# Optimization experiments

Hardware: AMD Instinct MI355X
Metric: run time of the kernel (lower is better)

The kernel has to match this reference:

```python
import jax, jax.numpy as jnp
import numpy as np

CLASS_W = jnp.array([0.3, 3.0, 0.3], dtype=jnp.float32)
GAMMA = 2.0
DICE_SMOOTH = 1.0
SKEL_SMOOTH = 1.0
W_FD, W_SK, W_B = 0.3, 0.3, 0.2
BIG = 1e8  # > max possible squared distance (3*63^2), keeps values finite


def _sq_edt(feature):
    """Exact squared Euclidean distance to nearest True voxel, separable
    per-axis (Felzenszwalb-style lower envelope realized as a brute-force
    min over each line, fully vectorized). feature: bool [B,D,H,W]."""
    d2 = jnp.where(feature, 0.0, BIG).astype(jnp.float32)
    for ax in range(1, d2.ndim):
        L = d2.shape[ax]
        i = jnp.arange(L, dtype=jnp.float32)
        cost = (i[:, None] - i[None, :]) ** 2  # [L, L]
        m = jnp.moveaxis(d2, ax, -1)           # [..., L]
        m = jnp.min(m[..., None, :] + cost, axis=-1)
        d2 = jnp.moveaxis(m, -1, ax)
    return d2


def setup_inputs() -> dict:
    key = jax.random.key(0)
    k1, k2, k3 = jax.random.split(key, 3)
    logits = jax.random.normal(k1, (4, 3, 64, 64, 64), dtype=jnp.float32)
    targets = jax.random.randint(k2, (4, 64, 64, 64), 0, 3, dtype=jnp.int64)
    skeleton = jax.random.randint(k3, (4, 64, 64, 64), 0, 2, dtype=jnp.int32)
    return {"logits": logits, "targets": targets, "skeleton": skeleton}


def reference(logits, targets, skeleton):
    num_classes = logits.shape[1]
    log_p = jax.nn.log_softmax(logits, axis=1)
    probs = jnp.exp(log_p)

    # ---- focal loss ----
    tgt = targets[:, None]  # [B,1,D,H,W]
    p_t = jnp.take_along_axis(probs, tgt, axis=1)[:, 0]
    log_p_t = jnp.take_along_axis(log_p, tgt, axis=1)[:, 0]
    alpha_t = CLASS_W[targets]
    focal = -(alpha_t * (1.0 - p_t) ** GAMMA * log_p_t).mean()

    # ---- dice loss (weighted, per class) ----
    dice = 0.0
    for c in range(num_classes):
        p = probs[:, c]
        t = (targets == c).astype(jnp.float32)
        inter = (p * t).sum()
        union = p.sum() + t.sum()
        dice = dice + CLASS_W[c] * (1.0 - (2.0 * inter + DICE_SMOOTH) / (union + DICE_SMOOTH))
    lfd = focal + dice / CLASS_W.sum()

    # ---- skeleton recall ----
    pred = probs[:, 1]  # surface class
    skel = skeleton.astype(jnp.float32)
    lsk = 1.0 - ((pred * skel).sum() + SKEL_SMOOTH) / (skel.sum() + SKEL_SMOOTH)

    # ---- boundary (signed distance transform) loss ----
    gt = targets == 1
    dt_pos = jnp.sqrt(_sq_edt(gt))    # dist to nearest gt==1
    dt_neg = jnp.sqrt(_sq_edt(~gt))   # dist to nearest gt==0
    signed = dt_pos - dt_neg
    B = gt.shape[0]
    nvox = gt[0].size
    gsum = gt.reshape(B, -1).sum(axis=1)
    mean_pred = pred.mean(axis=(1, 2, 3))
    term = (pred * signed).mean(axis=(1, 2, 3))
    per_b = jnp.where(gsum == 0, mean_pred,
                      jnp.where(gsum == nvox, 1.0 - mean_pred, term))
    lb = per_b.mean()

    total = W_FD * lfd + W_SK * lsk + W_B * lb
    return total, lfd, lsk, lb
```

## Files before the change

### kernel.cpp

```cpp
#include <hip/hip_runtime.h>
#include <math.h>

#define VOXB 262144
#define NVOX 1048576
#define NACC 11
#define PITCH 65
#define NBLKB 256
#define CLAMP14 16383

__device__ __forceinline__ unsigned pk_min(unsigned a, unsigned b) {
    unsigned d; asm("v_pk_min_u16 %0, %1, %2" : "=v"(d) : "v"(a), "v"(b)); return d;
}
__device__ __forceinline__ unsigned pk_max(unsigned a, unsigned b) {
    unsigned d; asm("v_pk_max_u16 %0, %1, %2" : "=v"(d) : "v"(a), "v"(b)); return d;
}
__device__ __forceinline__ unsigned pk_add(unsigned a, unsigned b) {
    unsigned d; asm("v_pk_add_u16 %0, %1, %2" : "=v"(d) : "v"(a), "v"(b)); return d;
}

__device__ __forceinline__ unsigned n2i(unsigned long long m, int i) {
    unsigned long long right = m >> i;
    unsigned long long left  = m << (63 - i);
    int dr = right ? __builtin_ctzll(right) : 1000;
    int dl = left  ? __builtin_clzll(left)  : 1000;
    int d  = dr < dl ? dr : dl;
    int d2 = d * d;
    return (unsigned)(d2 > CLAMP14 ? CLAMP14 : d2);
}

__global__ __launch_bounds__(512) void build_masks(
        const int* __restrict__ targets, unsigned long long* __restrict__ Mask) {
    __shared__ unsigned long long Mp[8][64];
    int slab = blockIdx.x;
    int b = slab >> 6, h = slab & 63;
    int wv = threadIdx.x >> 6, lane = threadIdx.x & 63;
    int base = b * VOXB + h * 64 + lane;
    unsigned long long bits = 0;
#pragma unroll
    for (int rt = 0; rt < 8; ++rt) {
        int d = wv * 8 + rt;
        int tv = targets[base + d * 4096];
        bits |= ((unsigned long long)(tv == 1)) << d;
    }
    Mp[wv][lane] = bits;
    __syncthreads();
    if (wv == 0) {
        unsigned long long m = Mp[0][lane] | Mp[1][lane] | Mp[2][lane] |
                               Mp[3][lane] | Mp[4][lane] | Mp[5][lane] |
                               Mp[6][lane] | Mp[7][lane];
        Mask[slab * 64 + lane] = m;
    }
}

__device__ __forceinline__ void vox_accum(float l0, float l1, float l2,
                                          int tg, int s, float sd, float* acc) {
    float m  = fmaxf(l0, fmaxf(l1, l2));
    float e0 = __expf(l0 - m), e1 = __expf(l1 - m), e2 = __expf(l2 - m);
    float sum = e0 + e1 + e2;
    float inv = 1.0f / sum;
    float p0 = e0 * inv, p1 = e1 * inv, p2 = e2 * inv;
    float logs = __logf(sum);
    float pt, lpt, alpha;
    if (tg == 0)      { pt = p0; lpt = l0 - m - logs; alpha = 0.3f; }
    else if (tg == 1) { pt = p1; lpt = l1 - m - logs; alpha = 3.0f; }
    else              { pt = p2; lpt = l2 - m - logs; alpha = 0.3f; }
    float om = 1.0f - pt;
    acc[0] += alpha * om * om * lpt;
    acc[1] += (tg == 0) ? p0 : 0.f;
    acc[2] += (tg == 1) ? p1 : 0.f;
    acc[3] += (tg == 2) ? p2 : 0.f;
    acc[4] += p1; acc[5] += p2;
    acc[6] += (tg == 1) ? 1.f : 0.f;
    acc[7] += (tg == 2) ? 1.f : 0.f;
    float fs = (float)s;
    acc[8] += p1 * fs;
    acc[9] += fs;
    acc[10] += p1 * sd;
}

__global__ __launch_bounds__(1024) void edt_reduce(
        const float* __restrict__ logits, const int* __restrict__ targets,
        const int* __restrict__ skel, const unsigned long long* __restrict__ Mask,
        float* __restrict__ partials) {
    __shared__ union {
        struct {
            unsigned long long Msk[4096];
            unsigned int V0[4096];
            unsigned int T[64 * PITCH];
        } a;
        float red[NACC * 1024];
    } S;
    int plane = blockIdx.x;
    int b = plane >> 6, d0 = plane & 63;
    int t = threadIdx.x;
    int wv = t >> 6, lane = t & 63;
    int hbase = wv * 4;

    int pbase = b * VOXB + d0 * 4096;
    int   tv[4], sv[4];
    float l0[4], l1[4], l2[4];
    size_t lbase = (size_t)b * (3 * VOXB) + d0 * 4096;
#pragma unroll
    for (int rt = 0; rt < 4; ++rt) {
        int off = pbase + (hbase + rt) * 64 + lane;
        tv[rt] = targets[off];
        sv[rt] = skel[off];
        size_t lb = lbase + (hbase + rt) * 64 + lane;
        l0[rt] = logits[lb];
        l1[rt] = logits[lb + VOXB];
        l2[rt] = logits[lb + 2 * VOXB];
    }

#pragma unroll
    for (int k = 0; k < 4; ++k)
        S.a.Msk[k * 1024 + t] = Mask[b * 4096 + k * 1024 + t];
    __syncthreads();

    unsigned mp[4];
#pragma unroll
    for (int rt = 0; rt < 4; ++rt) {
        unsigned long long m = S.a.Msk[(hbase + rt) * 64 + lane];
        unsigned v = n2i(m, d0) | (n2i(~m, d0) << 16);
        S.a.V0[(hbase + rt) * 64 + lane] = v;
        mp[rt] = v;
    }
    for (int r = 1; r < 64; ++r) {
        int jl = lane - r; jl = jl < 0 ? 0 : jl;
        int jr = lane + r; jr = jr > 63 ? 63 : jr;
        unsigned rr2 = (unsigned)(r * r) * 0x10001u;
        unsigned mx = 0;
#pragma unroll
        for (int rt = 0; rt < 4; ++rt) {
            unsigned a = S.a.V0[(hbase + rt) * 64 + jl];
            unsigned c = S.a.V0[(hbase + rt) * 64 + jr];
            mp[rt] = pk_min(mp[rt], pk_add(pk_min(a, c), rr2));
            mx = pk_max(mx, mp[rt]);
        }
        unsigned thr = (unsigned)((r + 1) * (r + 1));
        bool ok = ((mx & 0xffffu) <= thr) && ((mx >> 16) <= thr);
        if (__all(ok)) break;
    }
#pragma unroll
    for (int rt = 0; rt < 4; ++rt)
        S.a.T[lane * PITCH + hbase + rt] = pk_min(mp[rt], 0x3FFF3FFFu);
    __syncthreads();

    unsigned mh[4];
#pragma unroll
    for (int rt = 0; rt < 4; ++rt) mh[rt] = S.a.T[lane * PITCH + hbase + rt];
    for (int r = 1; r < 64; ++r) {
        unsigned rr2 = (unsigned)(r * r) * 0x10001u;
        unsigned mx = 0;
#pragma unroll
        for (int rt = 0; rt < 4; ++rt) {
            int h = hbase + rt;
            int jl = h - r; jl = jl < 0 ? 0 : jl;
            int jr = h + r; jr = jr > 63 ? 63 : jr;
            unsigned a = S.a.T[lane * PITCH + jl];
            unsigned c = S.a.T[lane * PITCH + jr];
            mh[rt] = pk_min(mh[rt], pk_add(pk_min(a, c), rr2));
            mx = pk_max(mx, mh[rt]);
        }
        unsigned thr = (unsigned)((r + 1) * (r + 1));
        bool ok = ((mx & 0xffffu) <= thr) && ((mx >> 16) <= thr);
        if (__all(ok)) break;
    }

    float acc[NACC];
#pragma unroll
    for (int k = 0; k < NACC; ++k) acc[k] = 0.f;
#pragma unroll
    for (int rt = 0; rt < 4; ++rt) {
        float sd = sqrtf((float)(mh[rt] & 0xffffu)) - sqrtf((float)(mh[rt] >> 16));
        vox_accum(l0[rt], l1[rt], l2[rt], tv[rt], sv[rt], sd, acc);
    }

    __syncthreads();
#pragma unroll
    for (int k = 0; k < NACC; ++k) S.red[k * 1024 + t] = acc[k];
    __syncthreads();
    if (wv < NACC) {
        const float* p = S.red + wv * 1024;
        float v = 0.f;
#pragma unroll
        for (int c = 0; c < 16; ++c) v += p[lane + c * 64];
#pragma unroll
        for (int off = 32; off; off >>= 1) v += __shfl_down(v, off, 64);
        if (lane == 0) partials[wv * NBLKB + blockIdx.x] = v;
    }
}

__global__ __launch_bounds__(256) void final_reduce(
        const float* __restrict__ partials, float* __restrict__ out) {
    __shared__ float sb[NACC][4];
    int w = threadIdx.x >> 6, lane = threadIdx.x & 63;
#pragma unroll
    for (int k = 0; k < NACC; ++k) {
        float v = partials[k * NBLKB + w * 64 + lane];
#pragma unroll
        for (int off = 32; off; off >>= 1) v += __shfl_down(v, off, 64);
        if (lane == 0) sb[k][w] = v;
    }
    __syncthreads();
    if (threadIdx.x == 0) {
        double S[NACC];
#pragma unroll
        for (int k = 0; k < NACC; ++k)
            S[k] = (double)sb[k][0] + sb[k][1] + sb[k][2] + sb[k][3];
        double psum0 = (double)NVOX - S[4] - S[5];
        double tsum0 = (double)NVOX - S[6] - S[7];
        double focal = -S[0] / (double)NVOX;
        double dice =
            0.3 * (1.0 - (2.0 * S[1] + 1.0) / (psum0 + tsum0 + 1.0)) +
            3.0 * (1.0 - (2.0 * S[2] + 1.0) / (S[4] + S[6] + 1.0)) +
            0.3 * (1.0 - (2.0 * S[3] + 1.0) / (S[5] + S[7] + 1.0));
        double lfd = focal + dice / 3.6;
        double lsk = 1.0 - (S[8] + 1.0) / (S[9] + 1.0);
        double lb = 0.0;
        for (int bb = 0; bb < 4; ++bb) {
            double gs = sb[6][bb];
            double ps = sb[4][bb];
            double tm = sb[10][bb];
            double per;
            if (gs == 0.0)               per = ps / (double)VOXB;
            else if (gs == (double)VOXB) per = 1.0 - ps / (double)VOXB;
            else                         per = tm / (double)VOXB;
            lb += per;
        }
        lb *= 0.25;
        double total = 0.3 * lfd + 0.3 * lsk + 0.2 * lb;
        out[0] = (float)total;
        out[1] = (float)lfd;
        out[2] = (float)lsk;
        out[3] = (float)lb;
    }
}

extern "C" void kernel_launch(void* const* d_in, const int* in_sizes, int n_in,
                              void* d_out, int out_size, void* d_ws, size_t ws_size,
                              hipStream_t stream) {
    const float* logits  = (const float*)d_in[0];
    const int*   targets = (const int*)d_in[1];
    const int*   skel    = (const int*)d_in[2];
    unsigned long long* Mask = (unsigned long long*)d_ws;
    float* partials = (float*)(Mask + 16384);
    float* out = (float*)d_out;

    build_masks<<<256, 512, 0, stream>>>(targets, Mask);
    edt_reduce<<<NBLKB, 1024, 0, stream>>>(logits, targets, skel, Mask, partials);
    final_reduce<<<1, 256, 0, stream>>>(partials, out);
}
```

Measured before the change: 24.83 us.

## Transpose EDT shared layout for vectorized LDS reads and drop mask staging

Each thread now loads its mask words straight from global memory into registers instead of staging them through shared memory, which removes one block barrier. The per-plane distance buffers are stored transposed with pitch 68, so every min-scan step fetches four neighbours with one 128-bit LDS read, for both the w and h passes. Global loads of logits, targets and skeleton become 128-bit vector loads along w, and barriers become a waitcnt plus s_barrier. In exchange, those global loads are strided by h across lanes, so coalescing is weaker, and the first pass relies on wave-local write-then-read ordering without a barrier.

```diff
diff --git a/kernel.cpp b/kernel.cpp
--- a/kernel.cpp
+++ b/kernel.cpp
@@ -4,7 +4,7 @@
 #define VOXB 262144
 #define NVOX 1048576
 #define NACC 11
-#define PITCH 65
+#define PITCH 68
 #define NBLKB 256
 #define CLAMP14 16383
 
@@ -26,6 +26,12 @@
     int d  = dr < dl ? dr : dl;
     int d2 = d * d;
     return (unsigned)(d2 > CLAMP14 ? CLAMP14 : d2);
+}
+
+__device__ __forceinline__ void lgkm_barrier() {
+    asm volatile("s_waitcnt lgkmcnt(0)" ::: "memory");
+    __builtin_amdgcn_s_barrier();
+    asm volatile("" ::: "memory");
 }
 
 __global__ __launch_bounds__(512) void build_masks(
@@ -82,105 +88,89 @@
         const float* __restrict__ logits, const int* __restrict__ targets,
         const int* __restrict__ skel, const unsigned long long* __restrict__ Mask,
         float* __restrict__ partials) {
-    __shared__ union {
-        struct {
-            unsigned long long Msk[4096];
-            unsigned int V0[4096];
-            unsigned int T[64 * PITCH];
-        } a;
-        float red[NACC * 1024];
-    } S;
+    __shared__ unsigned V0T[64 * PITCH];
+    __shared__ unsigned T2 [64 * PITCH];
+    __shared__ float red[NACC * 1024];
     int plane = blockIdx.x;
     int b = plane >> 6, d0 = plane & 63;
     int t = threadIdx.x;
     int wv = t >> 6, lane = t & 63;
-    int hbase = wv * 4;
-
-    int pbase = b * VOXB + d0 * 4096;
-    int   tv[4], sv[4];
-    float l0[4], l1[4], l2[4];
-    size_t lbase = (size_t)b * (3 * VOXB) + d0 * 4096;
-#pragma unroll
-    for (int rt = 0; rt < 4; ++rt) {
-        int off = pbase + (hbase + rt) * 64 + lane;
-        tv[rt] = targets[off];
-        sv[rt] = skel[off];
-        size_t lb = lbase + (hbase + rt) * 64 + lane;
-        l0[rt] = logits[lb];
-        l1[rt] = logits[lb + VOXB];
-        l2[rt] = logits[lb + 2 * VOXB];
-    }
-
-#pragma unroll
-    for (int k = 0; k < 4; ++k)
-        S.a.Msk[k * 1024 + t] = Mask[b * 4096 + k * 1024 + t];
-    __syncthreads();
+    int hbase = wv * 4, wbase = wv * 4;
+
+    const unsigned long long* mb = Mask + b * 4096;
+    unsigned long long mk[4];
+#pragma unroll
+    for (int rt = 0; rt < 4; ++rt) mk[rt] = mb[(hbase + rt) * 64 + lane];
+
+    int pbase = b * VOXB + d0 * 4096 + lane * 64 + wbase;
+    int4 tv4 = *reinterpret_cast<const int4*>(targets + pbase);
+    int4 sv4 = *reinterpret_cast<const int4*>(skel + pbase);
+    size_t lbase = (size_t)b * (3 * VOXB) + d0 * 4096 + lane * 64 + wbase;
+    float4 L0 = *reinterpret_cast<const float4*>(logits + lbase);
+    float4 L1 = *reinterpret_cast<const float4*>(logits + lbase + VOXB);
+    float4 L2 = *reinterpret_cast<const float4*>(logits + lbase + 2 * VOXB);
 
     unsigned mp[4];
 #pragma unroll
-    for (int rt = 0; rt < 4; ++rt) {
-        unsigned long long m = S.a.Msk[(hbase + rt) * 64 + lane];
-        unsigned v = n2i(m, d0) | (n2i(~m, d0) << 16);
-        S.a.V0[(hbase + rt) * 64 + lane] = v;
-        mp[rt] = v;
-    }
+    for (int rt = 0; rt < 4; ++rt)
+        mp[rt] = n2i(mk[rt], d0) | (n2i(~mk[rt], d0) << 16);
+    *reinterpret_cast<uint4*>(&V0T[lane * PITCH + hbase]) =
+        make_uint4(mp[0], mp[1], mp[2], mp[3]);
+
     for (int r = 1; r < 64; ++r) {
         int jl = lane - r; jl = jl < 0 ? 0 : jl;
         int jr = lane + r; jr = jr > 63 ? 63 : jr;
+        uint4 qa = *reinterpret_cast<const uint4*>(&V0T[jl * PITCH + hbase]);
+        uint4 qc = *reinterpret_cast<const uint4*>(&V0T[jr * PITCH + hbase]);
         unsigned rr2 = (unsigned)(r * r) * 0x10001u;
-        unsigned mx = 0;
-#pragma unroll
-        for (int rt = 0; rt < 4; ++rt) {
-            unsigned a = S.a.V0[(hbase + rt) * 64 + jl];
-            unsigned c = S.a.V0[(hbase + rt) * 64 + jr];
-            mp[rt] = pk_min(mp[rt], pk_add(pk_min(a, c), rr2));
-            mx = pk_max(mx, mp[rt]);
-        }
+        unsigned mx;
+        mp[0] = pk_min(mp[0], pk_add(pk_min(qa.x, qc.x), rr2)); mx = mp[0];
+        mp[1] = pk_min(mp[1], pk_add(pk_min(qa.y, qc.y), rr2)); mx = pk_max(mx, mp[1]);
+        mp[2] = pk_min(mp[2], pk_add(pk_min(qa.z, qc.z), rr2)); mx = pk_max(mx, mp[2]);
+        mp[3] = pk_min(mp[3], pk_add(pk_min(qa.w, qc.w), rr2)); mx = pk_max(mx, mp[3]);
         unsigned thr = (unsigned)((r + 1) * (r + 1));
-        bool ok = ((mx & 0xffffu) <= thr) && ((mx >> 16) <= thr);
-        if (__all(ok)) break;
-    }
-#pragma unroll
-    for (int rt = 0; rt < 4; ++rt)
-        S.a.T[lane * PITCH + hbase + rt] = pk_min(mp[rt], 0x3FFF3FFFu);
-    __syncthreads();
-
-    unsigned mh[4];
-#pragma unroll
-    for (int rt = 0; rt < 4; ++rt) mh[rt] = S.a.T[lane * PITCH + hbase + rt];
+        if (__all(((mx & 0xffffu) <= thr) && ((mx >> 16) <= thr))) break;
+    }
+#pragma unroll
+    for (int rt = 0; rt < 4; ++rt) T2[(hbase + rt) * PITCH + lane] = mp[rt];
+    lgkm_barrier();
+
+    uint4 q0 = *reinterpret_cast<const uint4*>(&T2[lane * PITCH + wbase]);
+    unsigned mh[4] = {q0.x, q0.y, q0.z, q0.w};
     for (int r = 1; r < 64; ++r) {
+        int jl = lane - r; jl = jl < 0 ? 0 : jl;
+        int jr = lane + r; jr = jr > 63 ? 63 : jr;
+        uint4 qa = *reinterpret_cast<const uint4*>(&T2[jl * PITCH + wbase]);
+        uint4 qc = *reinterpret_cast<const uint4*>(&T2[jr * PITCH + wbase]);
         unsigned rr2 = (unsigned)(r * r) * 0x10001u;
-        unsigned mx = 0;
-#pragma unroll
-        for (int rt = 0; rt < 4; ++rt) {
-            int h = hbase + rt;
-            int jl = h - r; jl = jl < 0 ? 0 : jl;
-            int jr = h + r; jr = jr > 63 ? 63 : jr;
-            unsigned a = S.a.T[lane * PITCH + jl];
-            unsigned c = S.a.T[lane * PITCH + jr];
-            mh[rt] = pk_min(mh[rt], pk_add(pk_min(a, c), rr2));
-            mx = pk_max(mx, mh[rt]);
-        }
+        unsigned mx;
+        mh[0] = pk_min(mh[0], pk_add(pk_min(qa.x, qc.x), rr2)); mx = mh[0];
+        mh[1] = pk_min(mh[1], pk_add(pk_min(qa.y, qc.y), rr2)); mx = pk_max(mx, mh[1]);
+        mh[2] = pk_min(mh[2], pk_add(pk_min(qa.z, qc.z), rr2)); mx = pk_max(mx, mh[2]);
+        mh[3] = pk_min(mh[3], pk_add(pk_min(qa.w, qc.w), rr2)); mx = pk_max(mx, mh[3]);
         unsigned thr = (unsigned)((r + 1) * (r + 1));
-        bool ok = ((mx & 0xffffu) <= thr) && ((mx >> 16) <= thr);
-        if (__all(ok)) break;
+        if (__all(((mx & 0xffffu) <= thr) && ((mx >> 16) <= thr))) break;
     }
 
     float acc[NACC];
 #pragma unroll
     for (int k = 0; k < NACC; ++k) acc[k] = 0.f;
-#pragma unroll
-    for (int rt = 0; rt < 4; ++rt) {
-        float sd = sqrtf((float)(mh[rt] & 0xffffu)) - sqrtf((float)(mh[rt] >> 16));
-        vox_accum(l0[rt], l1[rt], l2[rt], tv[rt], sv[rt], sd, acc);
-    }
-
-    __syncthreads();
-#pragma unroll
-    for (int k = 0; k < NACC; ++k) S.red[k * 1024 + t] = acc[k];
-    __syncthreads();
+    {
+        float sd0 = sqrtf((float)(mh[0] & 0xffffu)) - sqrtf((float)(mh[0] >> 16));
+        float sd1 = sqrtf((float)(mh[1] & 0xffffu)) - sqrtf((float)(mh[1] >> 16));
+        float sd2 = sqrtf((float)(mh[2] & 0xffffu)) - sqrtf((float)(mh[2] >> 16));
+        float sd3 = sqrtf((float)(mh[3] & 0xffffu)) - sqrtf((float)(mh[3] >> 16));
+        vox_accum(L0.x, L1.x, L2.x, tv4.x, sv4.x, sd0, acc);
+        vox_accum(L0.y, L1.y, L2.y, tv4.y, sv4.y, sd1, acc);
+        vox_accum(L0.z, L1.z, L2.z, tv4.z, sv4.z, sd2, acc);
+        vox_accum(L0.w, L1.w, L2.w, tv4.w, sv4.w, sd3, acc);
+    }
+
+#pragma unroll
+    for (int k = 0; k < NACC; ++k) red[k * 1024 + t] = acc[k];
+    lgkm_barrier();
     if (wv < NACC) {
-        const float* p = S.red + wv * 1024;
+        const float* p = red + wv * 1024;
         float v = 0.f;
 #pragma unroll
         for (int c = 0; c < 16; ++c) v += p[lane + c * 64];
```

Result: no change. 24.48 us (-1.4%).
